# Kernel tuning notes

Hardware: AMD Instinct MI355X
Metric: run time of the kernel (lower is better)

The kernel has to match this reference:

```python
import jax, jax.numpy as jnp
import numpy as np

N = 8192
D = 256
E = 131072


def setup_inputs() -> dict:
    key = jax.random.key(0)
    k1, k2 = jax.random.split(key)
    l_enc = jax.random.normal(k1, (N, D), dtype=jnp.float32)
    edge_index = jax.random.randint(k2, (2, E), 0, N, dtype=jnp.int64)
    return {"l_enc": l_enc, "edge_index": edge_index}


def reference(l_enc, edge_index):
    n = l_enc.shape[0]
    dt = l_enc.dtype
    # Vectorized symmetric adjacency build (replaces the per-edge Python loop).
    adj = (
        jnp.zeros((n, n), dtype=dt)
        .at[edge_index[0], edge_index[1]].set(1.0)
        .at[edge_index[1], edge_index[0]].set(1.0)
    )
    # Dense Gram matrix + sigmoid, diagonal zeroed like (1 - eye) * res.
    res = jax.nn.sigmoid(jnp.matmul(l_enc, l_enc.T))
    mask = jnp.eye(n, dtype=dt)
    res = (1.0 - mask) * res
    # BCE with torch-style log clamp at -100 (handles res == 0 on the diagonal).
    log_p = jnp.maximum(jnp.log(res), -100.0)
    log_1mp = jnp.maximum(jnp.log1p(-res), -100.0)
    return jnp.mean(-(adj * log_p + (1.0 - adj) * log_1mp))
```

## Files before the change

### kernel.cpp

```cpp
#include <hip/hip_runtime.h>
#include <hip/hip_bf16.h>

#define NN 8192
#define DK 256
#define NE 131072
#define T128 64
#define NBLK (T128*(T128+1)/2)

typedef __attribute__((ext_vector_type(8))) short bf16x8;
typedef __attribute__((ext_vector_type(4))) float f32x4;
typedef const __attribute__((address_space(1))) void* gas1_t;
typedef __attribute__((address_space(3))) void* las3_t;

__device__ __align__(16) unsigned       g_mask[(size_t)NN*NN/32];
__device__ __align__(16) unsigned short g_bf[(size_t)NN*DK];
__device__ __align__(16) double g_part[NBLK];

__device__ __forceinline__ unsigned short f2bf(float f) {
    unsigned u = __float_as_uint(f);
    unsigned r = (u + 0x7FFFu + ((u >> 16) & 1u)) >> 16;
    return (unsigned short)r;
}

__global__ void k_convscat(const float* __restrict__ x,
                           const long long* __restrict__ ei) {
    int i = blockIdx.x * 256 + threadIdx.x;
    float4 v = ((const float4*)x)[i];
    ushort4 b;
    b.x = f2bf(v.x); b.y = f2bf(v.y); b.z = f2bf(v.z); b.w = f2bf(v.w);
    *(ushort4*)(&g_bf[(size_t)i * 4]) = b;
    if (blockIdx.x < NE / 256) {
        int e = blockIdx.x * 256 + threadIdx.x;
        int ii = (int)ei[e];
        int jj = (int)ei[NE + e];
        atomicOr(&g_mask[(size_t)ii * (NN/32) + (jj >> 5)], 1u << (jj & 31));
        atomicOr(&g_mask[(size_t)jj * (NN/32) + (ii >> 5)], 1u << (ii & 31));
    }
}

__global__ __launch_bounds__(256, 3) void k_loss() {
    __shared__ __align__(16) unsigned short lsA[128 * 64];
    __shared__ __align__(16) unsigned short lsB[128 * 64];
    __shared__ double s_part[4];

    int orig = blockIdx.x;
    int bid  = (orig & 7) * (NBLK / 8) + (orig >> 3);
    int rem = bid, ti = 0;
    while (rem >= T128 - ti) { rem -= T128 - ti; ++ti; }
    int tj = ti + rem;

    const int tid  = threadIdx.x;
    const int lane = tid & 63;
    const int w    = tid >> 6;
    const int wr   = w >> 1;
    const int wc   = w & 1;
    const int lr   = lane & 15;
    const int lq   = lane >> 4;

    const int gq = (tid & 7) ^ ((tid >> 3) & 7);
    const unsigned short* srcA0 = g_bf + (size_t)(ti * 128 + (tid >> 3)) * DK + gq * 8;
    const size_t dB = (size_t)(tj - ti) * 128 * DK;
    const int lds0 = tid * 8;

#define STAGE(kt) do {                                                             \
    _Pragma("unroll")                                                              \
    for (int i = 0; i < 4; ++i) {                                                  \
        __builtin_amdgcn_global_load_lds(                                          \
            (gas1_t)(const void*)(srcA0 + (size_t)i * 32 * DK + (kt) * 64),        \
            (las3_t)(void*)&lsA[lds0 + i * 2048], 16, 0, 0);                       \
        __builtin_amdgcn_global_load_lds(                                          \
            (gas1_t)(const void*)(srcA0 + dB + (size_t)i * 32 * DK + (kt) * 64),   \
            (las3_t)(void*)&lsB[lds0 + i * 2048], 16, 0, 0);                       \
    }                                                                              \
} while (0)

    f32x4 acc[4][4] = {};

    STAGE(0);
    __syncthreads();

    #pragma unroll
    for (int kt = 0; kt < 4; ++kt) {
        #pragma unroll
        for (int ks = 0; ks < 2; ++ks) {
            const int cq = (ks * 4 + lq) ^ (lr & 7);
            bf16x8 fa[4];
            #pragma unroll
            for (int fm = 0; fm < 4; ++fm) {
                int ra = wr * 64 + fm * 16 + lr;
                fa[fm] = *(const bf16x8*)((const char*)&lsA[0] + ra * 128 + cq * 16);
            }
            #pragma unroll
            for (int fn = 0; fn < 4; ++fn) {
                int rb = wc * 64 + fn * 16 + lr;
                bf16x8 fbv = *(const bf16x8*)((const char*)&lsB[0] + rb * 128 + cq * 16);
                #pragma unroll
                for (int fm = 0; fm < 4; ++fm)
                    acc[fm][fn] = __builtin_amdgcn_mfma_f32_16x16x32_bf16(
                        fa[fm], fbv, acc[fm][fn], 0, 0, 0);
            }
        }
        if (kt < 3) {
            __syncthreads();
            STAGE(kt + 1);
            __syncthreads();
        }
    }
#undef STAGE

    const int R0 = ti * 128 + wr * 64;
    const int C0 = tj * 128 + wc * 64;
    const char* mrow0 = (const char*)g_mask + (size_t)(C0 >> 5) * 4;
    const bool diagB = (ti == tj) && (wr == wc);
    float tsum = 0.0f;
    #pragma unroll
    for (int fm = 0; fm < 4; ++fm) {
        #pragma unroll
        for (int r2 = 0; r2 < 4; ++r2) {
            int rowg = R0 + fm * 16 + lq * 4 + r2;
            uint2 m2 = *(const uint2*)(mrow0 + (size_t)rowg * (NN / 8));
            #pragma unroll
            for (int fn = 0; fn < 4; ++fn) {
                float s = acc[fm][fn][r2];
                unsigned mw = (fn & 2) ? m2.y : m2.x;
                bool bit = ((mw >> ((fn & 1) * 16 + lr)) & 1) != 0;
                float x  = bit ? -s : s;
                float wv = x * 1.44269504f;
                float e2 = __builtin_amdgcn_exp2f(fminf(wv, 126.0f));
                float t  = 0.6931471805599453f * __builtin_amdgcn_logf(1.0f + e2);
                float thr = bit ? 128.0f : 24.0f;
                float term = (wv >= thr) ? 100.0f : t;
                if (diagB && fm == fn && (lq * 4 + r2) == lr)
                    term = bit ? 100.0f : 0.0f;
                tsum += term;
            }
        }
    }
    #pragma unroll
    for (int off = 32; off; off >>= 1) tsum += __shfl_down(tsum, off);
    if (lane == 0) {
        float wgt = (ti == tj) ? 1.0f : 2.0f;
        s_part[w] = (double)(tsum * wgt);
    }
    __syncthreads();
    if (tid == 0)
        g_part[orig] = (s_part[0] + s_part[1]) + (s_part[2] + s_part[3]);
}

__global__ void k_final(const long long* __restrict__ ei, float* __restrict__ out) {
    int e = blockIdx.x * 256 + threadIdx.x;
    if (e < NE) {
        int ii = (int)ei[e];
        int jj = (int)ei[NE + e];
        g_mask[(size_t)ii * (NN/32) + (jj >> 5)] = 0u;
        g_mask[(size_t)jj * (NN/32) + (ii >> 5)] = 0u;
    }
    if (blockIdx.x == 0) {
        __shared__ double sd[256];
        double s = 0.0;
        for (int i = threadIdx.x; i < NBLK; i += 256) s += g_part[i];
        sd[threadIdx.x] = s;
        __syncthreads();
        #pragma unroll
        for (int st = 128; st; st >>= 1) {
            if (threadIdx.x < st) sd[threadIdx.x] += sd[threadIdx.x + st];
            __syncthreads();
        }
        if (threadIdx.x == 0)
            out[0] = (float)(sd[0] * (1.0 / ((double)NN * (double)NN)));
    }
}

extern "C" void kernel_launch(void* const* d_in, const int* in_sizes, int n_in,
                              void* d_out, int out_size, void* d_ws, size_t ws_size,
                              hipStream_t stream) {
    const float* l_enc = (const float*)d_in[0];
    const long long* ei = (const long long*)d_in[1];
    float* out = (float*)d_out;

    k_convscat<<<2048, 256, 0, stream>>>(l_enc, ei);
    k_loss<<<NBLK, 256, 0, stream>>>();
    k_final<<<NE / 256, 256, 0, stream>>>(ei, out);
}
```

Before: 58.78 us.

## Use 512-thread blocks with 8 waves per 128x128 tile and fold ln2 scaling

The loss kernel now runs 8 waves per 128x128 output tile instead of 4. Each wave computes a 64x32 subtile with half the accumulators, and each thread issues half as many staging loads. The epilogue works in log2 units, applies the ln2 factor once per block in double precision, and drops the exp clamp. This lowers register pressure and raises parallelism per tile. In exchange it adds more waves per block, more synchronisation and less MFMA work per wave.

```diff
diff --git a/kernel.cpp b/kernel.cpp
--- a/kernel.cpp
+++ b/kernel.cpp
@@ -6,6 +6,9 @@
 #define NE 131072
 #define T128 64
 #define NBLK (T128*(T128+1)/2)
+#define L2E 1.44269504f
+#define SAT_L2 144.269504f
+#define LN2D 0.6931471805599453
 
 typedef __attribute__((ext_vector_type(8))) short bf16x8;
 typedef __attribute__((ext_vector_type(4))) float f32x4;
@@ -38,10 +41,10 @@
     }
 }
 
-__global__ __launch_bounds__(256, 3) void k_loss() {
+__global__ __launch_bounds__(512, 4) void k_loss() {
     __shared__ __align__(16) unsigned short lsA[128 * 64];
     __shared__ __align__(16) unsigned short lsB[128 * 64];
-    __shared__ double s_part[4];
+    __shared__ double s_part[8];
 
     int orig = blockIdx.x;
     int bid  = (orig & 7) * (NBLK / 8) + (orig >> 3);
@@ -52,8 +55,8 @@
     const int tid  = threadIdx.x;
     const int lane = tid & 63;
     const int w    = tid >> 6;
-    const int wr   = w >> 1;
-    const int wc   = w & 1;
+    const int wr   = w >> 2;
+    const int wc   = w & 3;
     const int lr   = lane & 15;
     const int lq   = lane >> 4;
 
@@ -64,17 +67,17 @@
 
 #define STAGE(kt) do {                                                             \
     _Pragma("unroll")                                                              \
-    for (int i = 0; i < 4; ++i) {                                                  \
+    for (int i = 0; i < 2; ++i) {                                                  \
         __builtin_amdgcn_global_load_lds(                                          \
-            (gas1_t)(const void*)(srcA0 + (size_t)i * 32 * DK + (kt) * 64),        \
-            (las3_t)(void*)&lsA[lds0 + i * 2048], 16, 0, 0);                       \
+            (gas1_t)(const void*)(srcA0 + (size_t)i * 64 * DK + (kt) * 64),        \
+            (las3_t)(void*)&lsA[lds0 + i * 4096], 16, 0, 0);                       \
         __builtin_amdgcn_global_load_lds(                                          \
-            (gas1_t)(const void*)(srcA0 + dB + (size_t)i * 32 * DK + (kt) * 64),   \
-            (las3_t)(void*)&lsB[lds0 + i * 2048], 16, 0, 0);                       \
+            (gas1_t)(const void*)(srcA0 + dB + (size_t)i * 64 * DK + (kt) * 64),   \
+            (las3_t)(void*)&lsB[lds0 + i * 4096], 16, 0, 0);                       \
     }                                                                              \
 } while (0)
 
-    f32x4 acc[4][4] = {};
+    f32x4 acc[4][2] = {};
 
     STAGE(0);
     __syncthreads();
@@ -91,8 +94,8 @@
                 fa[fm] = *(const bf16x8*)((const char*)&lsA[0] + ra * 128 + cq * 16);
             }
             #pragma unroll
-            for (int fn = 0; fn < 4; ++fn) {
-                int rb = wc * 64 + fn * 16 + lr;
+            for (int fn = 0; fn < 2; ++fn) {
+                int rb = wc * 32 + fn * 16 + lr;
                 bf16x8 fbv = *(const bf16x8*)((const char*)&lsB[0] + rb * 128 + cq * 16);
                 #pragma unroll
                 for (int fm = 0; fm < 4; ++fm)
@@ -109,42 +112,42 @@
 #undef STAGE
 
     const int R0 = ti * 128 + wr * 64;
-    const int C0 = tj * 128 + wc * 64;
-    const char* mrow0 = (const char*)g_mask + (size_t)(C0 >> 5) * 4;
-    const bool diagB = (ti == tj) && (wr == wc);
+    const int mcol = tj * 4 + wc;
+    const bool dtile = (ti == tj);
     float tsum = 0.0f;
     #pragma unroll
     for (int fm = 0; fm < 4; ++fm) {
         #pragma unroll
         for (int r2 = 0; r2 < 4; ++r2) {
-            int rowg = R0 + fm * 16 + lq * 4 + r2;
-            uint2 m2 = *(const uint2*)(mrow0 + (size_t)rowg * (NN / 8));
+            int rl   = wr * 64 + fm * 16 + lq * 4 + r2;
+            unsigned mw = g_mask[(size_t)(ti * 128 + rl) * (NN/32) + mcol];
             #pragma unroll
-            for (int fn = 0; fn < 4; ++fn) {
+            for (int fn = 0; fn < 2; ++fn) {
                 float s = acc[fm][fn][r2];
-                unsigned mw = (fn & 2) ? m2.y : m2.x;
-                bool bit = ((mw >> ((fn & 1) * 16 + lr)) & 1) != 0;
-                float x  = bit ? -s : s;
-                float wv = x * 1.44269504f;
-                float e2 = __builtin_amdgcn_exp2f(fminf(wv, 126.0f));
-                float t  = 0.6931471805599453f * __builtin_amdgcn_logf(1.0f + e2);
+                int cl  = wc * 32 + fn * 16 + lr;
+                bool bit = ((mw >> (fn * 16 + lr)) & 1) != 0;
+                float wv = s * L2E;
+                float aw = bit ? -wv : wv;
+                float e2 = __builtin_amdgcn_exp2f(aw);
+                float l  = __builtin_amdgcn_logf(1.0f + e2);
                 float thr = bit ? 128.0f : 24.0f;
-                float term = (wv >= thr) ? 100.0f : t;
-                if (diagB && fm == fn && (lq * 4 + r2) == lr)
-                    term = bit ? 100.0f : 0.0f;
+                float term = (aw >= thr) ? SAT_L2 : l;
+                if (dtile && rl == cl)
+                    term = bit ? SAT_L2 : 0.0f;
                 tsum += term;
             }
         }
     }
     #pragma unroll
     for (int off = 32; off; off >>= 1) tsum += __shfl_down(tsum, off);
-    if (lane == 0) {
-        float wgt = (ti == tj) ? 1.0f : 2.0f;
-        s_part[w] = (double)(tsum * wgt);
+    if (lane == 0) s_part[w] = (double)tsum;
+    __syncthreads();
+    if (tid == 0) {
+        double acc8 = ((s_part[0] + s_part[1]) + (s_part[2] + s_part[3]))
+                    + ((s_part[4] + s_part[5]) + (s_part[6] + s_part[7]));
+        double wgt = (ti == tj) ? LN2D : 2.0 * LN2D;
+        g_part[orig] = acc8 * wgt;
     }
-    __syncthreads();
-    if (tid == 0)
-        g_part[orig] = (s_part[0] + s_part[1]) + (s_part[2] + s_part[3]);
 }
 
 __global__ void k_final(const long long* __restrict__ ei, float* __restrict__ out) {
@@ -179,6 +182,6 @@
     float* out = (float*)d_out;
 
     k_convscat<<<2048, 256, 0, stream>>>(l_enc, ei);
-    k_loss<<<NBLK, 256, 0, stream>>>();
+    k_loss<<<NBLK, 512, 0, stream>>>();
     k_final<<<NE / 256, 256, 0, stream>>>(ei, out);
 }
```

After: 58.80 us. About the same (+0.0%).
